# Kernel tuning notes

Measured on AMD Instinct MI355X. Metric: run time of the kernel, lower is better.

## Reference

```python
import math
import jax, jax.numpy as jnp
import numpy as np

B, N, D_IN, D_OUT = 8, 2048, 768, 768

def setup_inputs() -> dict:
    key = jax.random.key(0)
    k1, k2, k3 = jax.random.split(key, 3)
    x = jax.random.normal(k1, (B, N, D_IN), dtype=jnp.float32)
    W_qkv = jax.random.normal(k2, (D_IN, 3 * D_OUT), dtype=jnp.float32) * (1.0 / math.sqrt(D_IN))
    b_qkv = jax.random.normal(k3, (3 * D_OUT,), dtype=jnp.float32) * 0.02
    return {"x": x, "W_qkv": W_qkv, "b_qkv": b_qkv}

def reference(x, W_qkv, b_qkv):
    d_out = D_OUT
    # fused QKV projection: [B, N, 3*d_out]
    qkv = jnp.einsum('bnd,de->bne', x, W_qkv) + b_qkv
    q = qkv[:, :, :d_out]
    k = qkv[:, :, d_out:2 * d_out]
    v = qkv[:, :, 2 * d_out:3 * d_out]
    scale = 1.0 / math.sqrt(d_out)
    # scores: [B, N, N]
    scores = jnp.einsum('bqd,bkd->bqk', q, k) * scale
    attn = jax.nn.softmax(scores, axis=-1)
    # context: [B, N, d_out]
    context = jnp.einsum('bqk,bkd->bqd', attn, v)
    return context
```

## Files before the change

### kernel.cpp

```cpp
#include <hip/hip_runtime.h>
#include <hip/hip_bf16.h>

typedef __attribute__((ext_vector_type(8))) short short8;
typedef __attribute__((ext_vector_type(4))) float floatx4;

#define BATCH 8
#define SEQ 2048
#define DMODEL 768
#define NQKV 2304
#define SCALE 0.03608439182435161f

__device__ __forceinline__ ushort f2bf(float f) {
    union { float f; uint u; } in; in.f = f;
    uint u = in.u;
    return (ushort)((u + 0x7FFFu + ((u >> 16) & 1u)) >> 16);
}
__device__ __forceinline__ float bf2f(ushort h) {
    union { uint u; float f; } o; o.u = ((uint)h) << 16;
    return o.f;
}

__device__ __forceinline__ void async_copy16(void* lds_uniform, const void* gaddr) {
    __builtin_amdgcn_global_load_lds(
        (const __attribute__((address_space(1))) void*)gaddr,
        (__attribute__((address_space(3))) void*)lds_uniform,
        16, 0, 0);
}

__device__ __forceinline__ void stage128x32(ushort* lds, const ushort* gbase,
                                            size_t ld, int k0, int wave, int lane) {
    #pragma unroll
    for (int t = 0; t < 2; ++t) {
        const int chunk = wave * 2 + t;
        const int row = chunk * 16 + (lane >> 2);
        const ushort* g = gbase + (size_t)row * ld + k0 + (lane & 3) * 8;
        async_copy16(lds + chunk * 512, g);
    }
}

__global__ __launch_bounds__(256) void convert_x(const float* __restrict__ X,
                                                 ushort* __restrict__ Xb) {
    const int total = (BATCH * SEQ * DMODEL) / 8;
    for (int i = blockIdx.x * 256 + threadIdx.x; i < total; i += gridDim.x * 256) {
        const float4 v0 = reinterpret_cast<const float4*>(X)[(size_t)i * 2];
        const float4 v1 = reinterpret_cast<const float4*>(X)[(size_t)i * 2 + 1];
        uint4 u;
        u.x = (uint)f2bf(v0.x) | ((uint)f2bf(v0.y) << 16);
        u.y = (uint)f2bf(v0.z) | ((uint)f2bf(v0.w) << 16);
        u.z = (uint)f2bf(v1.x) | ((uint)f2bf(v1.y) << 16);
        u.w = (uint)f2bf(v1.z) | ((uint)f2bf(v1.w) << 16);
        reinterpret_cast<uint4*>(Xb)[i] = u;
    }
}

__global__ __launch_bounds__(256) void convert_wt(const float* __restrict__ W,
                                                  ushort* __restrict__ Wt) {
    __shared__ float tile[32][33];
    const int n0 = blockIdx.x * 32, k0 = blockIdx.y * 32;
    const int tx = threadIdx.x & 31, ty = threadIdx.x >> 5;
    #pragma unroll
    for (int i = 0; i < 32; i += 8)
        tile[ty + i][tx] = W[(size_t)(k0 + ty + i) * NQKV + n0 + tx];
    __syncthreads();
    #pragma unroll
    for (int i = 0; i < 32; i += 8)
        Wt[(size_t)(n0 + ty + i) * DMODEL + k0 + tx] = f2bf(tile[tx][ty + i]);
}

__global__ __launch_bounds__(256) void transpose_v(const ushort* __restrict__ Vb,
                                                   ushort* __restrict__ Vt) {
    __shared__ ushort tile[32][33];
    const int b = blockIdx.z;
    const int n0 = blockIdx.x * 32, d0 = blockIdx.y * 32;
    const ushort* src = Vb + (size_t)b * SEQ * DMODEL;
    ushort* dst = Vt + (size_t)b * DMODEL * SEQ;
    const int tx = threadIdx.x & 31, ty = threadIdx.x >> 5;
    #pragma unroll
    for (int i = 0; i < 32; i += 8)
        tile[ty + i][tx] = src[(size_t)(n0 + ty + i) * DMODEL + d0 + tx];
    __syncthreads();
    #pragma unroll
    for (int i = 0; i < 32; i += 8)
        dst[(size_t)(d0 + ty + i) * SEQ + n0 + tx] = tile[tx][ty + i];
}

__global__ __launch_bounds__(256) void qkv_gemm(
    const ushort* __restrict__ Xb,
    const ushort* __restrict__ Wt,
    const float* __restrict__ bias,
    ushort* __restrict__ Qs, ushort* __restrict__ Kb, ushort* __restrict__ Vb)
{
    __shared__ ushort As[128 * 32];
    __shared__ ushort Bs[128 * 32];
    const int tid  = threadIdx.x;
    const int m0   = blockIdx.x * 128, n0 = blockIdx.y * 128;
    const int wave = tid >> 6, lane = tid & 63;
    const int wm   = (wave >> 1) * 64, wn = (wave & 1) * 64;
    const int lr   = lane & 15, kg = lane >> 4;
    const ushort* Abase = Xb + (size_t)m0 * DMODEL;
    const ushort* Bbase = Wt + (size_t)n0 * DMODEL;
    floatx4 acc[4][4] = {};

    for (int k0 = 0; k0 < DMODEL; k0 += 32) {
        stage128x32(As, Abase, DMODEL, k0, wave, lane);
        stage128x32(Bs, Bbase, DMODEL, k0, wave, lane);
        __syncthreads();
        short8 a[4], b[4];
        #pragma unroll
        for (int i = 0; i < 4; ++i)
            a[i] = *reinterpret_cast<const short8*>(&As[(wm + i * 16 + lr) * 32 + kg * 8]);
        #pragma unroll
        for (int j = 0; j < 4; ++j)
            b[j] = *reinterpret_cast<const short8*>(&Bs[(wn + j * 16 + lr) * 32 + kg * 8]);
        #pragma unroll
        for (int i = 0; i < 4; ++i)
            #pragma unroll
            for (int j = 0; j < 4; ++j)
                acc[i][j] = __builtin_amdgcn_mfma_f32_16x16x32_bf16(a[i], b[j], acc[i][j], 0, 0, 0);
        __syncthreads();
    }

    #pragma unroll
    for (int i = 0; i < 4; ++i) {
        #pragma unroll
        for (int r = 0; r < 4; ++r) {
            int m = m0 + wm + i * 16 + kg * 4 + r;
            #pragma unroll
            for (int j = 0; j < 4; ++j) {
                int e = n0 + wn + j * 16 + lr;
                float val = acc[i][j][r] + bias[e];
                if (e < DMODEL)
                    Qs[(size_t)m * DMODEL + e] = f2bf(val * SCALE);
                else if (e < 2 * DMODEL)
                    Kb[(size_t)m * DMODEL + (e - DMODEL)] = f2bf(val);
                else
                    Vb[(size_t)m * DMODEL + (e - 2 * DMODEL)] = f2bf(val);
            }
        }
    }
}

__global__ __launch_bounds__(256) void score_gemm(
    const ushort* __restrict__ Qs, const ushort* __restrict__ Kb,
    ushort* __restrict__ S)
{
    __shared__ ushort As[128 * 32];
    __shared__ ushort Bs[128 * 32];
    const int tid  = threadIdx.x;
    const int b    = blockIdx.z;
    const int m0   = blockIdx.x * 128, n0 = blockIdx.y * 128;
    const ushort* Abase = Qs + (size_t)(b * SEQ + m0) * DMODEL;
    const ushort* Bbase = Kb + (size_t)(b * SEQ + n0) * DMODEL;
    ushort* Sb = S + (size_t)b * SEQ * SEQ;
    const int wave = tid >> 6, lane = tid & 63;
    const int wm   = (wave >> 1) * 64, wn = (wave & 1) * 64;
    const int lr   = lane & 15, kg = lane >> 4;
    floatx4 acc[4][4] = {};

    for (int k0 = 0; k0 < DMODEL; k0 += 32) {
        stage128x32(As, Abase, DMODEL, k0, wave, lane);
        stage128x32(Bs, Bbase, DMODEL, k0, wave, lane);
        __syncthreads();
        short8 a[4], b2[4];
        #pragma unroll
        for (int i = 0; i < 4; ++i)
            a[i] = *reinterpret_cast<const short8*>(&As[(wm + i * 16 + lr) * 32 + kg * 8]);
        #pragma unroll
        for (int j = 0; j < 4; ++j)
            b2[j] = *reinterpret_cast<const short8*>(&Bs[(wn + j * 16 + lr) * 32 + kg * 8]);
        #pragma unroll
        for (int i = 0; i < 4; ++i)
            #pragma unroll
            for (int j = 0; j < 4; ++j)
                acc[i][j] = __builtin_amdgcn_mfma_f32_16x16x32_bf16(a[i], b2[j], acc[i][j], 0, 0, 0);
        __syncthreads();
    }

    #pragma unroll
    for (int i = 0; i < 4; ++i)
        #pragma unroll
        for (int r = 0; r < 4; ++r) {
            int m = m0 + wm + i * 16 + kg * 4 + r;
            #pragma unroll
            for (int j = 0; j < 4; ++j) {
                int n = n0 + wn + j * 16 + lr;
                Sb[(size_t)m * SEQ + n] = f2bf(acc[i][j][r]);
            }
        }
}

__global__ __launch_bounds__(256) void softmax_rows(ushort* __restrict__ S) {
    const int row = blockIdx.x;
    ushort* p = S + (size_t)row * SEQ;
    const int tid = threadIdx.x;
    const int wave = tid >> 6, lane = tid & 63;

    short8 v8 = *reinterpret_cast<const short8*>(p + tid * 8);
    float v[8];
    #pragma unroll
    for (int j = 0; j < 8; ++j) v[j] = bf2f((ushort)v8[j]);
    float mx = v[0];
    #pragma unroll
    for (int j = 1; j < 8; ++j) mx = fmaxf(mx, v[j]);
    #pragma unroll
    for (int off = 32; off >= 1; off >>= 1) mx = fmaxf(mx, __shfl_xor(mx, off));
    __shared__ float redm[4], reds[4];
    if (lane == 0) redm[wave] = mx;
    __syncthreads();
    mx = fmaxf(fmaxf(redm[0], redm[1]), fmaxf(redm[2], redm[3]));

    float e[8], s = 0.f;
    #pragma unroll
    for (int j = 0; j < 8; ++j) { e[j] = __expf(v[j] - mx); s += e[j]; }
    #pragma unroll
    for (int off = 32; off >= 1; off >>= 1) s += __shfl_xor(s, off);
    if (lane == 0) reds[wave] = s;
    __syncthreads();
    s = reds[0] + reds[1] + reds[2] + reds[3];
    float inv = 1.f / s;

    short8 o;
    #pragma unroll
    for (int j = 0; j < 8; ++j) o[j] = (short)f2bf(e[j] * inv);
    *reinterpret_cast<short8*>(p + tid * 8) = o;
}

__global__ __launch_bounds__(256) void pv_gemm(
    const ushort* __restrict__ P, const ushort* __restrict__ Vt,
    float* __restrict__ Out)
{
    __shared__ ushort As[128 * 32];
    __shared__ ushort Bs[128 * 32];
    const int tid  = threadIdx.x;
    const int b    = blockIdx.z;
    const int m0   = blockIdx.x * 128, n0 = blockIdx.y * 128;
    const ushort* Abase = P + (size_t)b * SEQ * SEQ + (size_t)m0 * SEQ;
    const ushort* Bbase = Vt + (size_t)b * DMODEL * SEQ + (size_t)n0 * SEQ;
    const int wave = tid >> 6, lane = tid & 63;
    const int wm   = (wave >> 1) * 64, wn = (wave & 1) * 64;
    const int lr   = lane & 15, kg = lane >> 4;
    floatx4 acc[4][4] = {};

    for (int k0 = 0; k0 < SEQ; k0 += 32) {
        stage128x32(As, Abase, SEQ, k0, wave, lane);
        stage128x32(Bs, Bbase, SEQ, k0, wave, lane);
        __syncthreads();
        short8 a[4], b2[4];
        #pragma unroll
        for (int i = 0; i < 4; ++i)
            a[i] = *reinterpret_cast<const short8*>(&As[(wm + i * 16 + lr) * 32 + kg * 8]);
        #pragma unroll
        for (int j = 0; j < 4; ++j)
            b2[j] = *reinterpret_cast<const short8*>(&Bs[(wn + j * 16 + lr) * 32 + kg * 8]);
        #pragma unroll
        for (int i = 0; i < 4; ++i)
            #pragma unroll
            for (int j = 0; j < 4; ++j)
                acc[i][j] = __builtin_amdgcn_mfma_f32_16x16x32_bf16(a[i], b2[j], acc[i][j], 0, 0, 0);
        __syncthreads();
    }

    #pragma unroll
    for (int i = 0; i < 4; ++i)
        #pragma unroll
        for (int r = 0; r < 4; ++r) {
            int m = m0 + wm + i * 16 + kg * 4 + r;
            #pragma unroll
            for (int j = 0; j < 4; ++j) {
                int n = n0 + wn + j * 16 + lr;
                Out[((size_t)b * SEQ + m) * DMODEL + n] = acc[i][j][r];
            }
        }
}

extern "C" void kernel_launch(void* const* d_in, const int* in_sizes, int n_in,
                              void* d_out, int out_size, void* d_ws, size_t ws_size,
                              hipStream_t stream) {
    const float* X    = (const float*)d_in[0];
    const float* W    = (const float*)d_in[1];
    const float* bias = (const float*)d_in[2];
    float* Out = (float*)d_out;

    char* ws = (char*)d_ws;
    ushort* S  = (ushort*)ws;
    ushort* Xb = (ushort*)ws;
    ushort* Wt = (ushort*)(ws + (size_t)BATCH * SEQ * DMODEL * 2);
    ushort* Qs = (ushort*)(ws + (size_t)BATCH * SEQ * SEQ * 2);
    ushort* Kb = Qs + (size_t)BATCH * SEQ * DMODEL;
    ushort* Vb = Kb + (size_t)BATCH * SEQ * DMODEL;
    ushort* Vt = Vb + (size_t)BATCH * SEQ * DMODEL;

    convert_x<<<2048, 256, 0, stream>>>(X, Xb);
    convert_wt<<<dim3(NQKV / 32, DMODEL / 32), 256, 0, stream>>>(W, Wt);
    qkv_gemm<<<dim3(128, 18), 256, 0, stream>>>(Xb, Wt, bias, Qs, Kb, Vb);
    transpose_v<<<dim3(SEQ / 32, DMODEL / 32, BATCH), 256, 0, stream>>>(Vb, Vt);
    score_gemm<<<dim3(16, 16, 8), 256, 0, stream>>>(Qs, Kb, S);
    softmax_rows<<<BATCH * SEQ, 256, 0, stream>>>(S);
    pv_gemm<<<dim3(16, 6, 8), 256, 0, stream>>>(S, Vt, Out);
}
```

Measured before the change: 298.1 us.

## Double K-tile depth to 64 with XOR-swizzled LDS layout in all GEMMs

All three GEMM kernels now stage 128x64 tiles per iteration instead of 128x32, which halves the number of barrier pairs and loop iterations. The global-to-LDS copy places 16-byte chunks at an XOR-swizzled column position (chunk index XOR row mod 8), and the MFMA operand reads apply the matching swizzle. This is meant to avoid LDS bank conflicts on the wider 64-element rows. LDS use per block doubles to 32KB, which may reduce occupancy.

```diff
diff --git a/kernel.cpp b/kernel.cpp
--- a/kernel.cpp
+++ b/kernel.cpp
@@ -27,13 +27,15 @@
         16, 0, 0);
 }
 
-__device__ __forceinline__ void stage128x32(ushort* lds, const ushort* gbase,
+__device__ __forceinline__ void stage128x64(ushort* lds, const ushort* gbase,
                                             size_t ld, int k0, int wave, int lane) {
-    #pragma unroll
-    for (int t = 0; t < 2; ++t) {
-        const int chunk = wave * 2 + t;
-        const int row = chunk * 16 + (lane >> 2);
-        const ushort* g = gbase + (size_t)row * ld + k0 + (lane & 3) * 8;
+    const int sub = lane >> 3;
+    const int cc  = (lane & 7) ^ sub;
+    #pragma unroll
+    for (int t = 0; t < 4; ++t) {
+        const int chunk = wave * 4 + t;
+        const int row   = chunk * 8 + sub;
+        const ushort* g = gbase + (size_t)row * ld + k0 + cc * 8;
         async_copy16(lds + chunk * 512, g);
     }
 }
@@ -84,39 +86,45 @@
         dst[(size_t)(d0 + ty + i) * SEQ + n0 + tx] = tile[tx][ty + i];
 }
 
+
 __global__ __launch_bounds__(256) void qkv_gemm(
     const ushort* __restrict__ Xb,
     const ushort* __restrict__ Wt,
     const float* __restrict__ bias,
     ushort* __restrict__ Qs, ushort* __restrict__ Kb, ushort* __restrict__ Vb)
 {
-    __shared__ ushort As[128 * 32];
-    __shared__ ushort Bs[128 * 32];
+    __shared__ ushort As[128 * 64];
+    __shared__ ushort Bs[128 * 64];
     const int tid  = threadIdx.x;
     const int m0   = blockIdx.x * 128, n0 = blockIdx.y * 128;
     const int wave = tid >> 6, lane = tid & 63;
     const int wm   = (wave >> 1) * 64, wn = (wave & 1) * 64;
     const int lr   = lane & 15, kg = lane >> 4;
+    const int xr   = lr & 7;
     const ushort* Abase = Xb + (size_t)m0 * DMODEL;
     const ushort* Bbase = Wt + (size_t)n0 * DMODEL;
     floatx4 acc[4][4] = {};
 
-    for (int k0 = 0; k0 < DMODEL; k0 += 32) {
-        stage128x32(As, Abase, DMODEL, k0, wave, lane);
-        stage128x32(Bs, Bbase, DMODEL, k0, wave, lane);
-        __syncthreads();
-        short8 a[4], b[4];
-        #pragma unroll
-        for (int i = 0; i < 4; ++i)
-            a[i] = *reinterpret_cast<const short8*>(&As[(wm + i * 16 + lr) * 32 + kg * 8]);
-        #pragma unroll
-        for (int j = 0; j < 4; ++j)
-            b[j] = *reinterpret_cast<const short8*>(&Bs[(wn + j * 16 + lr) * 32 + kg * 8]);
-        #pragma unroll
-        for (int i = 0; i < 4; ++i)
+    for (int k0 = 0; k0 < DMODEL; k0 += 64) {
+        stage128x64(As, Abase, DMODEL, k0, wave, lane);
+        stage128x64(Bs, Bbase, DMODEL, k0, wave, lane);
+        __syncthreads();
+        #pragma unroll
+        for (int ks = 0; ks < 2; ++ks) {
+            const int slot = ((ks * 4 + kg) ^ xr) * 8;
+            short8 a[4], b[4];
+            #pragma unroll
+            for (int i = 0; i < 4; ++i)
+                a[i] = *reinterpret_cast<const short8*>(&As[(wm + i * 16 + lr) * 64 + slot]);
             #pragma unroll
             for (int j = 0; j < 4; ++j)
-                acc[i][j] = __builtin_amdgcn_mfma_f32_16x16x32_bf16(a[i], b[j], acc[i][j], 0, 0, 0);
+                b[j] = *reinterpret_cast<const short8*>(&Bs[(wn + j * 16 + lr) * 64 + slot]);
+            #pragma unroll
+            for (int i = 0; i < 4; ++i)
+                #pragma unroll
+                for (int j = 0; j < 4; ++j)
+                    acc[i][j] = __builtin_amdgcn_mfma_f32_16x16x32_bf16(a[i], b[j], acc[i][j], 0, 0, 0);
+        }
         __syncthreads();
     }
 
@@ -144,8 +152,8 @@
     const ushort* __restrict__ Qs, const ushort* __restrict__ Kb,
     ushort* __restrict__ S)
 {
-    __shared__ ushort As[128 * 32];
-    __shared__ ushort Bs[128 * 32];
+    __shared__ ushort As[128 * 64];
+    __shared__ ushort Bs[128 * 64];
     const int tid  = threadIdx.x;
     const int b    = blockIdx.z;
     const int m0   = blockIdx.x * 128, n0 = blockIdx.y * 128;
@@ -155,24 +163,29 @@
     const int wave = tid >> 6, lane = tid & 63;
     const int wm   = (wave >> 1) * 64, wn = (wave & 1) * 64;
     const int lr   = lane & 15, kg = lane >> 4;
+    const int xr   = lr & 7;
     floatx4 acc[4][4] = {};
 
-    for (int k0 = 0; k0 < DMODEL; k0 += 32) {
-        stage128x32(As, Abase, DMODEL, k0, wave, lane);
-        stage128x32(Bs, Bbase, DMODEL, k0, wave, lane);
-        __syncthreads();
-        short8 a[4], b2[4];
-        #pragma unroll
-        for (int i = 0; i < 4; ++i)
-            a[i] = *reinterpret_cast<const short8*>(&As[(wm + i * 16 + lr) * 32 + kg * 8]);
-        #pragma unroll
-        for (int j = 0; j < 4; ++j)
-            b2[j] = *reinterpret_cast<const short8*>(&Bs[(wn + j * 16 + lr) * 32 + kg * 8]);
-        #pragma unroll
-        for (int i = 0; i < 4; ++i)
+    for (int k0 = 0; k0 < DMODEL; k0 += 64) {
+        stage128x64(As, Abase, DMODEL, k0, wave, lane);
+        stage128x64(Bs, Bbase, DMODEL, k0, wave, lane);
+        __syncthreads();
+        #pragma unroll
+        for (int ks = 0; ks < 2; ++ks) {
+            const int slot = ((ks * 4 + kg) ^ xr) * 8;
+            short8 a[4], b2[4];
+            #pragma unroll
+            for (int i = 0; i < 4; ++i)
+                a[i] = *reinterpret_cast<const short8*>(&As[(wm + i * 16 + lr) * 64 + slot]);
             #pragma unroll
             for (int j = 0; j < 4; ++j)
-                acc[i][j] = __builtin_amdgcn_mfma_f32_16x16x32_bf16(a[i], b2[j], acc[i][j], 0, 0, 0);
+                b2[j] = *reinterpret_cast<const short8*>(&Bs[(wn + j * 16 + lr) * 64 + slot]);
+            #pragma unroll
+            for (int i = 0; i < 4; ++i)
+                #pragma unroll
+                for (int j = 0; j < 4; ++j)
+                    acc[i][j] = __builtin_amdgcn_mfma_f32_16x16x32_bf16(a[i], b2[j], acc[i][j], 0, 0, 0);
+        }
         __syncthreads();
     }
 
@@ -229,8 +242,8 @@
     const ushort* __restrict__ P, const ushort* __restrict__ Vt,
     float* __restrict__ Out)
 {
-    __shared__ ushort As[128 * 32];
-    __shared__ ushort Bs[128 * 32];
+    __shared__ ushort As[128 * 64];
+    __shared__ ushort Bs[128 * 64];
     const int tid  = threadIdx.x;
     const int b    = blockIdx.z;
     const int m0   = blockIdx.x * 128, n0 = blockIdx.y * 128;
@@ -239,24 +252,29 @@
     const int wave = tid >> 6, lane = tid & 63;
     const int wm   = (wave >> 1) * 64, wn = (wave & 1) * 64;
     const int lr   = lane & 15, kg = lane >> 4;
+    const int xr   = lr & 7;
     floatx4 acc[4][4] = {};
 
-    for (int k0 = 0; k0 < SEQ; k0 += 32) {
-        stage128x32(As, Abase, SEQ, k0, wave, lane);
-        stage128x32(Bs, Bbase, SEQ, k0, wave, lane);
-        __syncthreads();
-        short8 a[4], b2[4];
-        #pragma unroll
-        for (int i = 0; i < 4; ++i)
-            a[i] = *reinterpret_cast<const short8*>(&As[(wm + i * 16 + lr) * 32 + kg * 8]);
-        #pragma unroll
-        for (int j = 0; j < 4; ++j)
-            b2[j] = *reinterpret_cast<const short8*>(&Bs[(wn + j * 16 + lr) * 32 + kg * 8]);
-        #pragma unroll
-        for (int i = 0; i < 4; ++i)
+    for (int k0 = 0; k0 < SEQ; k0 += 64) {
+        stage128x64(As, Abase, SEQ, k0, wave, lane);
+        stage128x64(Bs, Bbase, SEQ, k0, wave, lane);
+        __syncthreads();
+        #pragma unroll
+        for (int ks = 0; ks < 2; ++ks) {
+            const int slot = ((ks * 4 + kg) ^ xr) * 8;
+            short8 a[4], b2[4];
+            #pragma unroll
+            for (int i = 0; i < 4; ++i)
+                a[i] = *reinterpret_cast<const short8*>(&As[(wm + i * 16 + lr) * 64 + slot]);
             #pragma unroll
             for (int j = 0; j < 4; ++j)
-                acc[i][j] = __builtin_amdgcn_mfma_f32_16x16x32_bf16(a[i], b2[j], acc[i][j], 0, 0, 0);
+                b2[j] = *reinterpret_cast<const short8*>(&Bs[(wn + j * 16 + lr) * 64 + slot]);
+            #pragma unroll
+            for (int i = 0; i < 4; ++i)
+                #pragma unroll
+                for (int j = 0; j < 4; ++j)
+                    acc[i][j] = __builtin_amdgcn_mfma_f32_16x16x32_bf16(a[i], b2[j], acc[i][j], 0, 0, 0);
+        }
         __syncthreads();
     }
 
```

New measurement: 282.4 us. 5.3% less time.

## Replace three GEMMs with 256x256 double-buffered 8-wave pipelined MFMA kernel

Applied to the files above, without the earlier changes.

Swaps the simple 128x128, 4-wave, single-buffered GEMMs for one templated 256x256, 8-wave kernel. It double-buffers 64-wide K tiles in 128KB of dynamic LDS, uses an XOR-swizzled LDS layout, and interleaves async global-to-LDS staging with MFMA quarters under explicit waitcnt, barrier and setprio control. The aim is more data reuse per tile, hiding global load latency, and fewer LDS bank conflicts. The cost is much less parallelism: the PV GEMM gets only 192 blocks and the score GEMM 512, which may leave CUs underused, and the hand-tuned waitcnt scheme is fragile.

```diff
diff --git a/kernel.cpp b/kernel.cpp
--- a/kernel.cpp
+++ b/kernel.cpp
@@ -27,15 +27,191 @@
         16, 0, 0);
 }
 
-__device__ __forceinline__ void stage128x32(ushort* lds, const ushort* gbase,
-                                            size_t ld, int k0, int wave, int lane) {
-    #pragma unroll
-    for (int t = 0; t < 2; ++t) {
-        const int chunk = wave * 2 + t;
-        const int row = chunk * 16 + (lane >> 2);
-        const ushort* g = gbase + (size_t)row * ld + k0 + (lane & 3) * 8;
-        async_copy16(lds + chunk * 512, g);
+#define BARRIER() asm volatile("s_barrier" ::: "memory")
+#define LGKM0()   do { asm volatile("s_waitcnt lgkmcnt(0)" ::: "memory"); \
+                       __builtin_amdgcn_sched_barrier(0); } while (0)
+#define LGKM_HINT() asm volatile("s_waitcnt lgkmcnt(8)" ::: "memory")
+#define VMCNT(n)  asm volatile("s_waitcnt vmcnt(" #n ")" ::: "memory")
+
+template<int MODE, int KT>
+__global__ __launch_bounds__(512, 2) void gemm8(
+    const ushort* __restrict__ A, const ushort* __restrict__ B,
+    const float* __restrict__ bias,
+    void* __restrict__ out0, void* __restrict__ out1, void* __restrict__ out2,
+    int lda, int ldb)
+{
+    extern __shared__ __align__(16) ushort lds[];
+    const int tid  = threadIdx.x;
+    const int w    = tid >> 6, lane = tid & 63;
+    const int wr   = w >> 2,  wc   = w & 3;
+    const int lr   = lane & 15, kg = lane >> 4;
+    const int srow = lane >> 3;
+    const int scc  = (lane & 7) ^ srow;
+
+    const int m0 = blockIdx.x * 256, n0 = blockIdx.y * 256;
+    const ushort* Abase;
+    const ushort* Bbase;
+    if (MODE == 0) {
+        Abase = A + (size_t)m0 * lda;
+        Bbase = B + (size_t)n0 * ldb;
+    } else if (MODE == 1) {
+        const int b = blockIdx.z;
+        Abase = A + ((size_t)(b * SEQ + m0)) * lda;
+        Bbase = B + ((size_t)(b * SEQ + n0)) * ldb;
+    } else {
+        const int b = blockIdx.z;
+        Abase = A + (size_t)b * SEQ * SEQ + (size_t)m0 * lda;
+        Bbase = B + (size_t)b * DMODEL * SEQ + (size_t)n0 * ldb;
     }
+
+    const ushort* At[2] = { lds,         lds + 32768 };
+    const ushort* Bt[2] = { lds + 16384, lds + 49152 };
+
+    #define STG(tile, mat, half) do { if ((tile) < KT) {                          \
+        ushort* sb_ = lds + (((tile) & 1) ? 32768 : 0) + ((mat) ? 16384 : 0);     \
+        const ushort* g_ = (mat) ? Bbase : Abase;                                 \
+        const size_t ld_ = (mat) ? (size_t)ldb : (size_t)lda;                     \
+        const int k0_ = (tile) << 6;                                              \
+        _Pragma("unroll")                                                         \
+        for (int t_ = 0; t_ < 2; ++t_) {                                          \
+            const int c8_ = (mat) ? ((w & 3) + ((w >> 2) << 3) + (t_ << 4) + ((half) << 2)) \
+                                  : (w + (t_ << 4) + ((half) << 3));              \
+            const int row_ = (c8_ << 3) + srow;                                   \
+            async_copy16(sb_ + c8_ * 512, g_ + (size_t)row_ * ld_ + k0_ + scc * 8); \
+        } } } while (0)
+
+    short8 af[4][2], bf[4][2];
+    floatx4 acc[8][4] = {};
+
+    #define LDFRAG(tp, row, c) \
+        (*reinterpret_cast<const short8*>(&(tp)[((row) << 6) + ((((c) ^ ((row) & 7))) << 3)]))
+
+    #define READ_A(bufi, mh) do {                                                 \
+        _Pragma("unroll") for (int mf_ = 0; mf_ < 4; ++mf_)                       \
+        _Pragma("unroll") for (int kk_ = 0; kk_ < 2; ++kk_)                       \
+            af[mf_][kk_] = LDFRAG(At[bufi], wr * 128 + ((mh) * 4 + mf_) * 16 + lr, kk_ * 4 + kg); \
+    } while (0)
+    #define READ_B(bufi, nh) do {                                                 \
+        _Pragma("unroll") for (int nf_ = 0; nf_ < 2; ++nf_)                       \
+        _Pragma("unroll") for (int kk_ = 0; kk_ < 2; ++kk_)                       \
+            bf[(nh) * 2 + nf_][kk_] = LDFRAG(Bt[bufi], wc * 64 + ((nh) * 2 + nf_) * 16 + lr, kk_ * 4 + kg); \
+    } while (0)
+    #define MFMA_Q(mh, nh) do {                                                   \
+        __builtin_amdgcn_s_setprio(1);                                            \
+        _Pragma("unroll") for (int mf_ = 0; mf_ < 4; ++mf_)                       \
+        _Pragma("unroll") for (int nf_ = 0; nf_ < 2; ++nf_)                       \
+        _Pragma("unroll") for (int kk_ = 0; kk_ < 2; ++kk_)                       \
+            acc[(mh) * 4 + mf_][(nh) * 2 + nf_] = __builtin_amdgcn_mfma_f32_16x16x32_bf16( \
+                af[mf_][kk_], bf[(nh) * 2 + nf_][kk_], acc[(mh) * 4 + mf_][(nh) * 2 + nf_], 0, 0, 0); \
+        __builtin_amdgcn_s_setprio(0);                                            \
+    } while (0)
+
+    STG(0, 0, 0); STG(0, 1, 0); STG(0, 1, 1); STG(0, 0, 1);
+    STG(1, 0, 0); STG(1, 1, 0); STG(1, 1, 1);
+    VMCNT(6);
+    BARRIER();
+
+    #pragma unroll 1
+    for (int it = 0; it < KT / 2; ++it) {
+        const int t = 2 * it;
+        const bool lastit = (it == KT / 2 - 1);
+        READ_A(0, 0); READ_B(0, 0);
+        STG(t + 1, 0, 1);
+        LGKM_HINT();
+        BARRIER(); LGKM0();
+        MFMA_Q(0, 0);
+        BARRIER();
+        READ_B(0, 1);
+        STG(t + 2, 0, 0);
+        BARRIER(); LGKM0();
+        MFMA_Q(0, 1);
+        BARRIER();
+        READ_A(0, 1);
+        STG(t + 2, 1, 0);
+        BARRIER(); LGKM0();
+        MFMA_Q(1, 0);
+        BARRIER();
+        STG(t + 2, 1, 1);
+        BARRIER();
+        MFMA_Q(1, 1);
+        if (lastit) { VMCNT(0); } else { VMCNT(6); }
+        BARRIER();
+        READ_A(1, 0); READ_B(1, 0);
+        STG(t + 2, 0, 1);
+        LGKM_HINT();
+        BARRIER(); LGKM0();
+        MFMA_Q(0, 0);
+        BARRIER();
+        READ_B(1, 1);
+        STG(t + 3, 0, 0);
+        BARRIER(); LGKM0();
+        MFMA_Q(0, 1);
+        BARRIER();
+        READ_A(1, 1);
+        STG(t + 3, 1, 0);
+        BARRIER(); LGKM0();
+        MFMA_Q(1, 0);
+        BARRIER();
+        STG(t + 3, 1, 1);
+        BARRIER();
+        MFMA_Q(1, 1);
+        VMCNT(6);
+        BARRIER();
+    }
+
+    const int mrow = m0 + wr * 128, ncol = n0 + wc * 64;
+    if (MODE == 0) {
+        ushort* Qs = (ushort*)out0;
+        ushort* Kb = (ushort*)out1;
+        ushort* Vb = (ushort*)out2;
+        #pragma unroll
+        for (int nf = 0; nf < 4; ++nf) {
+            const int e = ncol + nf * 16 + lr;
+            const float bv = bias[e];
+            const bool isQ = e < DMODEL, isK = !isQ && (e < 2 * DMODEL);
+            ushort* dst = isQ ? Qs : (isK ? Kb : Vb);
+            const int ec = isQ ? e : (isK ? e - DMODEL : e - 2 * DMODEL);
+            const float mul = isQ ? SCALE : 1.0f;
+            #pragma unroll
+            for (int mf = 0; mf < 8; ++mf)
+                #pragma unroll
+                for (int r = 0; r < 4; ++r) {
+                    const int m = mrow + mf * 16 + kg * 4 + r;
+                    dst[(size_t)m * DMODEL + ec] = f2bf((acc[mf][nf][r] + bv) * mul);
+                }
+        }
+    } else if (MODE == 1) {
+        ushort* Sb = (ushort*)out0 + (size_t)blockIdx.z * SEQ * SEQ;
+        #pragma unroll
+        for (int nf = 0; nf < 4; ++nf) {
+            const int n = ncol + nf * 16 + lr;
+            #pragma unroll
+            for (int mf = 0; mf < 8; ++mf)
+                #pragma unroll
+                for (int r = 0; r < 4; ++r) {
+                    const int m = mrow + mf * 16 + kg * 4 + r;
+                    Sb[(size_t)m * SEQ + n] = f2bf(acc[mf][nf][r]);
+                }
+        }
+    } else {
+        float* Ob = (float*)out0 + (size_t)blockIdx.z * SEQ * DMODEL;
+        #pragma unroll
+        for (int nf = 0; nf < 4; ++nf) {
+            const int n = ncol + nf * 16 + lr;
+            #pragma unroll
+            for (int mf = 0; mf < 8; ++mf)
+                #pragma unroll
+                for (int r = 0; r < 4; ++r) {
+                    const int m = mrow + mf * 16 + kg * 4 + r;
+                    Ob[(size_t)m * DMODEL + n] = acc[mf][nf][r];
+                }
+        }
+    }
+    #undef STG
+    #undef LDFRAG
+    #undef READ_A
+    #undef READ_B
+    #undef MFMA_Q
 }
 
 __global__ __launch_bounds__(256) void convert_x(const float* __restrict__ X,
@@ -84,111 +260,6 @@
         dst[(size_t)(d0 + ty + i) * SEQ + n0 + tx] = tile[tx][ty + i];
 }
 
-__global__ __launch_bounds__(256) void qkv_gemm(
-    const ushort* __restrict__ Xb,
-    const ushort* __restrict__ Wt,
-    const float* __restrict__ bias,
-    ushort* __restrict__ Qs, ushort* __restrict__ Kb, ushort* __restrict__ Vb)
-{
-    __shared__ ushort As[128 * 32];
-    __shared__ ushort Bs[128 * 32];
-    const int tid  = threadIdx.x;
-    const int m0   = blockIdx.x * 128, n0 = blockIdx.y * 128;
-    const int wave = tid >> 6, lane = tid & 63;
-    const int wm   = (wave >> 1) * 64, wn = (wave & 1) * 64;
-    const int lr   = lane & 15, kg = lane >> 4;
-    const ushort* Abase = Xb + (size_t)m0 * DMODEL;
-    const ushort* Bbase = Wt + (size_t)n0 * DMODEL;
-    floatx4 acc[4][4] = {};
-
-    for (int k0 = 0; k0 < DMODEL; k0 += 32) {
-        stage128x32(As, Abase, DMODEL, k0, wave, lane);
-        stage128x32(Bs, Bbase, DMODEL, k0, wave, lane);
-        __syncthreads();
-        short8 a[4], b[4];
-        #pragma unroll
-        for (int i = 0; i < 4; ++i)
-            a[i] = *reinterpret_cast<const short8*>(&As[(wm + i * 16 + lr) * 32 + kg * 8]);
-        #pragma unroll
-        for (int j = 0; j < 4; ++j)
-            b[j] = *reinterpret_cast<const short8*>(&Bs[(wn + j * 16 + lr) * 32 + kg * 8]);
-        #pragma unroll
-        for (int i = 0; i < 4; ++i)
-            #pragma unroll
-            for (int j = 0; j < 4; ++j)
-                acc[i][j] = __builtin_amdgcn_mfma_f32_16x16x32_bf16(a[i], b[j], acc[i][j], 0, 0, 0);
-        __syncthreads();
-    }
-
-    #pragma unroll
-    for (int i = 0; i < 4; ++i) {
-        #pragma unroll
-        for (int r = 0; r < 4; ++r) {
-            int m = m0 + wm + i * 16 + kg * 4 + r;
-            #pragma unroll
-            for (int j = 0; j < 4; ++j) {
-                int e = n0 + wn + j * 16 + lr;
-                float val = acc[i][j][r] + bias[e];
-                if (e < DMODEL)
-                    Qs[(size_t)m * DMODEL + e] = f2bf(val * SCALE);
-                else if (e < 2 * DMODEL)
-                    Kb[(size_t)m * DMODEL + (e - DMODEL)] = f2bf(val);
-                else
-                    Vb[(size_t)m * DMODEL + (e - 2 * DMODEL)] = f2bf(val);
-            }
-        }
-    }
-}
-
-__global__ __launch_bounds__(256) void score_gemm(
-    const ushort* __restrict__ Qs, const ushort* __restrict__ Kb,
-    ushort* __restrict__ S)
-{
-    __shared__ ushort As[128 * 32];
-    __shared__ ushort Bs[128 * 32];
-    const int tid  = threadIdx.x;
-    const int b    = blockIdx.z;
-    const int m0   = blockIdx.x * 128, n0 = blockIdx.y * 128;
-    const ushort* Abase = Qs + (size_t)(b * SEQ + m0) * DMODEL;
-    const ushort* Bbase = Kb + (size_t)(b * SEQ + n0) * DMODEL;
-    ushort* Sb = S + (size_t)b * SEQ * SEQ;
-    const int wave = tid >> 6, lane = tid & 63;
-    const int wm   = (wave >> 1) * 64, wn = (wave & 1) * 64;
-    const int lr   = lane & 15, kg = lane >> 4;
-    floatx4 acc[4][4] = {};
-
-    for (int k0 = 0; k0 < DMODEL; k0 += 32) {
-        stage128x32(As, Abase, DMODEL, k0, wave, lane);
-        stage128x32(Bs, Bbase, DMODEL, k0, wave, lane);
-        __syncthreads();
-        short8 a[4], b2[4];
-        #pragma unroll
-        for (int i = 0; i < 4; ++i)
-            a[i] = *reinterpret_cast<const short8*>(&As[(wm + i * 16 + lr) * 32 + kg * 8]);
-        #pragma unroll
-        for (int j = 0; j < 4; ++j)
-            b2[j] = *reinterpret_cast<const short8*>(&Bs[(wn + j * 16 + lr) * 32 + kg * 8]);
-        #pragma unroll
-        for (int i = 0; i < 4; ++i)
-            #pragma unroll
-            for (int j = 0; j < 4; ++j)
-                acc[i][j] = __builtin_amdgcn_mfma_f32_16x16x32_bf16(a[i], b2[j], acc[i][j], 0, 0, 0);
-        __syncthreads();
-    }
-
-    #pragma unroll
-    for (int i = 0; i < 4; ++i)
-        #pragma unroll
-        for (int r = 0; r < 4; ++r) {
-            int m = m0 + wm + i * 16 + kg * 4 + r;
-            #pragma unroll
-            for (int j = 0; j < 4; ++j) {
-                int n = n0 + wn + j * 16 + lr;
-                Sb[(size_t)m * SEQ + n] = f2bf(acc[i][j][r]);
-            }
-        }
-}
-
 __global__ __launch_bounds__(256) void softmax_rows(ushort* __restrict__ S) {
     const int row = blockIdx.x;
     ushort* p = S + (size_t)row * SEQ;
@@ -223,54 +294,6 @@
     #pragma unroll
     for (int j = 0; j < 8; ++j) o[j] = (short)f2bf(e[j] * inv);
     *reinterpret_cast<short8*>(p + tid * 8) = o;
-}
-
-__global__ __launch_bounds__(256) void pv_gemm(
-    const ushort* __restrict__ P, const ushort* __restrict__ Vt,
-    float* __restrict__ Out)
-{
-    __shared__ ushort As[128 * 32];
-    __shared__ ushort Bs[128 * 32];
-    const int tid  = threadIdx.x;
-    const int b    = blockIdx.z;
-    const int m0   = blockIdx.x * 128, n0 = blockIdx.y * 128;
-    const ushort* Abase = P + (size_t)b * SEQ * SEQ + (size_t)m0 * SEQ;
-    const ushort* Bbase = Vt + (size_t)b * DMODEL * SEQ + (size_t)n0 * SEQ;
-    const int wave = tid >> 6, lane = tid & 63;
-    const int wm   = (wave >> 1) * 64, wn = (wave & 1) * 64;
-    const int lr   = lane & 15, kg = lane >> 4;
-    floatx4 acc[4][4] = {};
-
-    for (int k0 = 0; k0 < SEQ; k0 += 32) {
-        stage128x32(As, Abase, SEQ, k0, wave, lane);
-        stage128x32(Bs, Bbase, SEQ, k0, wave, lane);
-        __syncthreads();
-        short8 a[4], b2[4];
-        #pragma unroll
-        for (int i = 0; i < 4; ++i)
-            a[i] = *reinterpret_cast<const short8*>(&As[(wm + i * 16 + lr) * 32 + kg * 8]);
-        #pragma unroll
-        for (int j = 0; j < 4; ++j)
-            b2[j] = *reinterpret_cast<const short8*>(&Bs[(wn + j * 16 + lr) * 32 + kg * 8]);
-        #pragma unroll
-        for (int i = 0; i < 4; ++i)
-            #pragma unroll
-            for (int j = 0; j < 4; ++j)
-                acc[i][j] = __builtin_amdgcn_mfma_f32_16x16x32_bf16(a[i], b2[j], acc[i][j], 0, 0, 0);
-        __syncthreads();
-    }
-
-    #pragma unroll
-    for (int i = 0; i < 4; ++i)
-        #pragma unroll
-        for (int r = 0; r < 4; ++r) {
-            int m = m0 + wm + i * 16 + kg * 4 + r;
-            #pragma unroll
-            for (int j = 0; j < 4; ++j) {
-                int n = n0 + wn + j * 16 + lr;
-                Out[((size_t)b * SEQ + m) * DMODEL + n] = acc[i][j][r];
-            }
-        }
 }
 
 extern "C" void kernel_launch(void* const* d_in, const int* in_sizes, int n_in,
@@ -290,11 +313,22 @@
     ushort* Vb = Kb + (size_t)BATCH * SEQ * DMODEL;
     ushort* Vt = Vb + (size_t)BATCH * SEQ * DMODEL;
 
+    const int LDSB = 131072;
+    (void)hipFuncSetAttribute((const void*)gemm8<0, 12>,
+                              hipFuncAttributeMaxDynamicSharedMemorySize, LDSB);
+    (void)hipFuncSetAttribute((const void*)gemm8<1, 12>,
+                              hipFuncAttributeMaxDynamicSharedMemorySize, LDSB);
+    (void)hipFuncSetAttribute((const void*)gemm8<2, 32>,
+                              hipFuncAttributeMaxDynamicSharedMemorySize, LDSB);
+
     convert_x<<<2048, 256, 0, stream>>>(X, Xb);
     convert_wt<<<dim3(NQKV / 32, DMODEL / 32), 256, 0, stream>>>(W, Wt);
-    qkv_gemm<<<dim3(128, 18), 256, 0, stream>>>(Xb, Wt, bias, Qs, Kb, Vb);
+    gemm8<0, 12><<<dim3(64, 9), 512, LDSB, stream>>>(
+        Xb, Wt, bias, Qs, Kb, Vb, DMODEL, DMODEL);
     transpose_v<<<dim3(SEQ / 32, DMODEL / 32, BATCH), 256, 0, stream>>>(Vb, Vt);
-    score_gemm<<<dim3(16, 16, 8), 256, 0, stream>>>(Qs, Kb, S);
+    gemm8<1, 12><<<dim3(8, 8, 8), 512, LDSB, stream>>>(
+        Qs, Kb, nullptr, S, nullptr, nullptr, DMODEL, DMODEL);
     softmax_rows<<<BATCH * SEQ, 256, 0, stream>>>(S);
-    pv_gemm<<<dim3(16, 6, 8), 256, 0, stream>>>(S, Vt, Out);
-}
+    gemm8<2, 32><<<dim3(8, 3, 8), 512, LDSB, stream>>>(
+        S, Vt, nullptr, Out, nullptr, nullptr, SEQ, SEQ);
+}
```

Result: faster. 267.4 us (-10.3%).
